# Optimization experiments

Hardware: AMD Instinct MI355X
Metric: run time of the kernel (lower is better)

The kernel has to match this reference:

```python
import math
import jax, jax.numpy as jnp
import numpy as np

# ---------------- static structure (mirrors CG_woFilter_cuda + MyBatchNormWeightMM) ----------------
LMAX = 4
TAUS = [16, 16, 16, 16, 16]          # t_F: input channels per degree l
T_O  = [16, 16, 16, 16, 16]          # output channels per degree l after weight matmul
BN_EPS = 1e-5

# all (l, l1, l2) triples with l2 <= l1 <= lmax and |l1-l2| <= l <= min(l1+l2, lmax), sorted by (l,l1,l2)
TRIPLES = sorted([(l, l1, l2)
                  for l1 in range(LMAX + 1)
                  for l2 in range(l1 + 1)
                  for l in range(l1 - l2, min(l1 + l2, LMAX) + 1)])

T_FF = [0] * (LMAX + 1)              # t_FF[l] = sum over triples of taus[l1]*taus[l2]
for (l, l1, l2) in TRIPLES:
    T_FF[l] += TAUS[l1] * TAUS[l2]

def _cg_coef(j1, m1, j2, m2, j, m):
    """Clebsch-Gordan coefficient <j1 m1 j2 m2 | j m> (Condon-Shortley)."""
    if m1 + m2 != m:
        return 0.0
    f = math.factorial
    if j < abs(j1 - j2) or j > j1 + j2:
        return 0.0
    pref = math.sqrt((2 * j + 1) * f(j + j1 - j2) * f(j - j1 + j2) * f(j1 + j2 - j) / f(j1 + j2 + j + 1))
    pref *= math.sqrt(f(j + m) * f(j - m) * f(j1 - m1) * f(j1 + m1) * f(j2 - m2) * f(j2 + m2))
    s = 0.0
    for k in range(0, j1 + j2 - j + 1):
        if (j1 - m1 - k) < 0 or (j2 + m2 - k) < 0 or (j - j2 + m1 + k) < 0 or (j - j1 - m2 + k) < 0:
            continue
        s += ((-1.0) ** k) / (f(k) * f(j1 + j2 - j - k) * f(j1 - m1 - k)
                              * f(j2 + m2 - k) * f(j - j2 + m1 + k) * f(j - j1 - m2 + k))
    return pref * s

def _cg_matrix(l, l1, l2):
    C = np.zeros((2 * l + 1, 2 * l1 + 1, 2 * l2 + 1), dtype=np.float32)
    for m in range(-l, l + 1):
        for m1 in range(-l1, l1 + 1):
            m2 = m - m1
            if -l2 <= m2 <= l2:
                C[m + l, m1 + l1, m2 + l2] = _cg_coef(l1, m1, l2, m2, l, m)
    return C

CG_MATS = {t: jnp.asarray(_cg_matrix(*t)) for t in TRIPLES}

M_IN = sum(TAUS[l] * (2 * l + 1) for l in range(LMAX + 1))      # 400
W_LEN = sum(T_FF[l] * T_O[l] for l in range(LMAX + 1))          # 172032


def setup_inputs() -> dict:
    key = jax.random.key(0)
    k1, k2 = jax.random.split(key)
    B = 256
    Fs = jax.random.normal(k1, (B, M_IN, 2), dtype=jnp.float32)
    W = jax.random.normal(k2, (W_LEN, 2), dtype=jnp.float32) * 0.05
    return {"Fs": Fs, "W": W}


def reference(Fs, W):
    B = Fs.shape[0]
    # split input into per-degree blocks: F_l [B, tau, 2l+1, 2]
    Fl, off = [], 0
    for l in range(LMAX + 1):
        n = TAUS[l] * (2 * l + 1)
        Fl.append(Fs[:, off:off + n, :].reshape(B, TAUS[l], 2 * l + 1, 2))
        off += n
    # sparse CG tensor product: per-triple complex outer product contracted with CG coefs
    frags = [[] for _ in range(LMAX + 1)]
    for (l, l1, l2) in TRIPLES:
        C = CG_MATS[(l, l1, l2)]                     # [2l+1, 2l1+1, 2l2+1]
        a, b = Fl[l1], Fl[l2]
        ar, ai = a[..., 0], a[..., 1]
        br, bi = b[..., 0], b[..., 1]
        rr = jnp.einsum('bip,bjq,mpq->bijm', ar, br, C)
        ii = jnp.einsum('bip,bjq,mpq->bijm', ai, bi, C)
        ri = jnp.einsum('bip,bjq,mpq->bijm', ar, bi, C)
        ir = jnp.einsum('bip,bjq,mpq->bijm', ai, br, C)
        fr = (rr - ii).reshape(B, -1, 2 * l + 1)     # channels flattened as c1*tau2 + c2 (t_offsets order)
        fi = (ri + ir).reshape(B, -1, 2 * l + 1)
        frags[l].append(jnp.stack([fr, fi], axis=-1))
    # per-degree fragment batchnorm + complex weight matmul (FN_WMM)
    outs, woff = [], 0
    for l in range(LMAX + 1):
        FF = jnp.concatenate(frags[l], axis=1)       # [B, t_FF, 2l+1, 2]
        var = jnp.mean(jnp.sum(FF * FF, axis=-1), axis=(0, 2))      # per-channel mean |z|^2
        FFn = FF / (jnp.sqrt(var)[None, :, None, None] + BN_EPS)
        n = T_FF[l] * T_O[l]
        Wl = W[woff:woff + n].reshape(T_O[l], T_FF[l], 2)
        woff += n
        wr, wi = Wl[..., 0], Wl[..., 1]
        xr, xi = FFn[..., 0], FFn[..., 1]
        yr = jnp.einsum('oc,bcm->bom', wr, xr) - jnp.einsum('oc,bcm->bom', wi, xi)
        yi = jnp.einsum('oc,bcm->bom', wr, xi) + jnp.einsum('oc,bcm->bom', wi, xr)
        outs.append(jnp.stack([yr, yi], axis=-1).reshape(B, T_O[l] * (2 * l + 1), 2))
    return jnp.concatenate(outs, axis=1)             # [B, sum t_O[l]*(2l+1), 2] = [B, 400, 2]
```

## Files before the change

kernel.cpp:

```cpp
#include <hip/hip_runtime.h>
#include <math.h>

#define NTRI 42
#define NCH  10752
#define B_SZ 256
#define AH_PL 172032

typedef float    f32x4 __attribute__((ext_vector_type(4)));
typedef _Float16 half8 __attribute__((ext_vector_type(8)));
typedef _Float16 half4 __attribute__((ext_vector_type(4)));
typedef _Float16 f16x2 __attribute__((ext_vector_type(2)));

constexpr int CT_L [NTRI]={0,0,0,0,0, 1,1,1,1,1,1,1,1, 2,2,2,2,2,2,2,2,2,2, 3,3,3,3,3,3,3,3,3,3, 4,4,4,4,4,4,4,4,4};
constexpr int CT_L1[NTRI]={0,1,2,3,4, 1,1,2,2,3,3,4,4, 1,2,2,2,3,3,3,4,4,4, 2,2,3,3,3,3,4,4,4,4, 2,3,3,3,4,4,4,4,4};
constexpr int CT_L2[NTRI]={0,1,2,3,4, 0,1,1,2,2,3,3,4, 1,0,1,2,1,2,3,2,3,4, 1,2,0,1,2,3,1,2,3,4, 2,1,2,3,0,1,2,3,4};
constexpr int CT_T [NTRI]={0,1,2,3,4, 0,1,2,3,4,5,6,7, 0,1,2,3,4,5,6,7,8,9, 0,1,2,3,4,5,6,7,8,9, 0,1,2,3,4,5,6,7,8};

constexpr int KL_t[5]    ={1280,2048,2560,2560,2304};
constexpr int GBASE_t[5] ={0,1280,3328,5888,8448};
constexpr int ROFF_t[5]  ={0,16,64,144,256};
constexpr int NM_t[5]    ={1,3,5,7,9};
constexpr int FFB_t[5]   ={0,327680,1900544,5177344,9764864};
#define FF_TOT 15073280
constexpr int PL_t[5]    ={0,5,29,79,149};
#define PART_PL 4096
#define PART_TOT (230*PART_PL)

__device__ const int   dCTL[NTRI]={0,0,0,0,0, 1,1,1,1,1,1,1,1, 2,2,2,2,2,2,2,2,2,2, 3,3,3,3,3,3,3,3,3,3, 4,4,4,4,4,4,4,4,4};
__device__ const int   dCTT[NTRI]={0,1,2,3,4, 0,1,2,3,4,5,6,7, 0,1,2,3,4,5,6,7,8,9, 0,1,2,3,4,5,6,7,8,9, 0,1,2,3,4,5,6,7,8};
__device__ const int   dK[5]   ={1280,2048,2560,2560,2304};
__device__ const int   dWOFF[5]={0,20480,53248,94208,135168};
__device__ const int   dNM[5]  ={1,3,5,7,9};
__device__ const int   dFFB[5] ={0,327680,1900544,5177344,9764864};
__device__ const int   dPL[5]  ={0,5,29,79,149};
__device__ const int   dGB[5]  ={0,1280,3328,5888,8448};
__device__ const int   dROFF[5]={0,16,64,144,256};
__device__ const int   dNT[5]  ={5,8,10,10,9};
__device__ const float dINV[5] ={1.f/256.f,1.f/768.f,1.f/1280.f,1.f/1792.f,1.f/2304.f};

__device__ float  g_varsum[NCH];
__device__ __align__(16) f16x2  g_ff[FF_TOT];
__device__ __align__(16) f16x2  g_ah[2*AH_PL];
__device__ float2 g_part[PART_TOT];

constexpr double cfact(int n){ double r=1.0; for(int i=2;i<=n;i++) r*=(double)i; return r; }
constexpr double csqrt_(double v){ double x = v>1.0? v:1.0; for(int i=0;i<80;i++) x = 0.5*(x+v/x); return x; }
constexpr double ccg(int j1,int m1,int j2,int m2,int j,int m){
    if(m1+m2!=m) return 0.0;
    double pref = csqrt_((2.0*j+1.0)*cfact(j+j1-j2)*cfact(j-j1+j2)*cfact(j1+j2-j)/cfact(j1+j2+j+1));
    pref *= csqrt_(cfact(j+m)*cfact(j-m)*cfact(j1-m1)*cfact(j1+m1)*cfact(j2-m2)*cfact(j2+m2));
    double s=0.0;
    for(int k=0;k<=j1+j2-j;k++){
        int a=j1-m1-k, bb=j2+m2-k, c=j-j2+m1+k, d=j-j1-m2+k;
        if(a<0||bb<0||c<0||d<0) continue;
        double term = 1.0/(cfact(k)*cfact(j1+j2-j-k)*cfact(a)*cfact(bb)*cfact(c)*cfact(d));
        s += (k&1)? -term : term;
    }
    return pref*s;
}
struct CG81 { float a[81]; };
constexpr CG81 makecg(int l,int l1,int l2){
    CG81 t{};
    const int n1=2*l1+1;
    for(int mi=0;mi<2*l+1;mi++)
        for(int p=0;p<n1;p++){
            const int m=mi-l, m1=p-l1, m2=m-m1;
            if(m2>=-l2 && m2<=l2) t.a[mi*n1+p]=(float)ccg(l1,m1,l2,m2,l,m);
        }
    return t;
}
template<int TR> struct CGC { static constexpr CG81 t = makecg(CT_L[TR],CT_L1[TR],CT_L2[TR]); };

template<int TR>
__device__ __forceinline__ void cg_pair(const float2* __restrict__ sF,
                                        int i, int j0,
                                        float2* __restrict__ ff0,
                                        float2* __restrict__ ff1){
    constexpr int L=CT_L[TR], L1=CT_L1[TR], L2=CT_L2[TR];
    constexpr int N1=2*L1+1, N2=2*L2+1, NM=2*L+1;
    float2 A[N1], B0[N2], B1[N2];
    #pragma unroll
    for(int p=0;p<N1;p++) A[p]=sF[ROFF_t[L1]+i*N1+p];
    #pragma unroll
    for(int q=0;q<N2;q++) B0[q]=sF[ROFF_t[L2]+j0*N2+q];
    #pragma unroll
    for(int q=0;q<N2;q++) B1[q]=sF[ROFF_t[L2]+(j0+1)*N2+q];
    #pragma unroll
    for(int mi=0;mi<NM;mi++){
        float aR0=0.f, aI0=0.f, aR1=0.f, aI1=0.f;
        const int pLo = (mi-L+L1-L2) > 0 ? (mi-L+L1-L2) : 0;
        const int pHi = (mi-L+L1+L2) < 2*L1 ? (mi-L+L1+L2) : 2*L1;
        #pragma unroll
        for(int p=0;p<N1;p++){
            if(p>=pLo && p<=pHi){
                const float c = CGC<TR>::t.a[mi*N1+p];
                if(c != 0.f){
                    const int q = mi - L - p + L1 + L2;
                    const float cax=c*A[p].x, cay=c*A[p].y;
                    const float2 b0=B0[q], b1=B1[q];
                    aR0 = fmaf(cax,b0.x,aR0); aR0 = fmaf(-cay,b0.y,aR0);
                    aI0 = fmaf(cax,b0.y,aI0); aI0 = fmaf( cay,b0.x,aI0);
                    aR1 = fmaf(cax,b1.x,aR1); aR1 = fmaf(-cay,b1.y,aR1);
                    aI1 = fmaf(cax,b1.y,aI1); aI1 = fmaf( cay,b1.x,aI1);
                }
            }
        }
        ff0[mi]=make_float2(aR0,aI0);
        ff1[mi]=make_float2(aR1,aI1);
    }
}

template<int TR>
__device__ __forceinline__ void cg_one(const float2* __restrict__ sF, int bq, int t){
    constexpr int L=CT_L[TR], NM=2*L+1, T=CT_T[TR], K=KL_t[L];
    constexpr int NMK=NM*K;
    const int half = t>>7, tt = t&127;
    const int ch0 = tt*2;
    const int i = ch0>>4, j0 = ch0&15;
    float n20=0.f, n21=0.f;
    #pragma unroll
    for(int b4=0;b4<4;b4++){
        const int slab = half*4+b4;
        const int b = bq*8 + slab;
        float2 ff0[NM], ff1[NM];
        cg_pair<TR>(sF + slab*400, i, j0, ff0, ff1);
        const int base = FFB_t[L] + b*NMK + T*256 + ch0;
        #pragma unroll
        for(int m=0;m<NM;m++){
            n20 = fmaf(ff0[m].x,ff0[m].x,n20); n20 = fmaf(ff0[m].y,ff0[m].y,n20);
            n21 = fmaf(ff1[m].x,ff1[m].x,n21); n21 = fmaf(ff1[m].y,ff1[m].y,n21);
            half4 h;
            h[0]=(_Float16)ff0[m].x; h[1]=(_Float16)ff0[m].y;
            h[2]=(_Float16)ff1[m].x; h[3]=(_Float16)ff1[m].y;
            *reinterpret_cast<half4*>(g_ff + base + m*K) = h;
        }
    }
    atomicAdd(&g_varsum[GBASE_t[L] + T*256 + ch0    ], n20);
    atomicAdd(&g_varsum[GBASE_t[L] + T*256 + ch0 + 1], n21);
}

template<int TR>
__device__ __forceinline__ void cg_disp(int tr, const float2* sF, int bq, int t){
    if constexpr (TR < NTRI){
        if(tr==TR) cg_one<TR>(sF,bq,t);
        else       cg_disp<TR+1>(tr,sF,bq,t);
    }
}

__global__ void __launch_bounds__(256) k_cg(const float2* __restrict__ Fs){
    __shared__ float4 sF4[1600];
    const int bq=blockIdx.y, t=threadIdx.x;
    const float4* __restrict__ F4 = reinterpret_cast<const float4*>(Fs) + bq*1600;
    #pragma unroll
    for(int k=0;k<6;k++) sF4[t + k*256] = F4[t + k*256];
    if(t<64) sF4[t+1536] = F4[t+1536];
    __syncthreads();
    cg_disp<0>(blockIdx.x, reinterpret_cast<const float2*>(sF4), bq, t);
}

__global__ void __launch_bounds__(256) k_wn(const float2* __restrict__ W2){
    const int tr=blockIdx.x, t=threadIdx.x;
    const int l=dCTL[tr], T=dCTT[tr], K=dK[l];
    const int ch = dGB[l] + T*256 + t;
    const float s = g_varsum[ch];
    g_varsum[ch] = 0.f;
    const float invv = 1.f/(sqrtf(s*dINV[l])+1e-5f);
    const int base = dWOFF[l] + T*256 + t;
    #pragma unroll 4
    for(int o=0;o<16;o++){
        const float2 w = W2[base + o*K];
        f16x2 hr, hi;
        hr.x=(_Float16)( w.x*invv); hr.y=(_Float16)(-w.y*invv);
        hi.x=(_Float16)( w.y*invv); hi.y=(_Float16)( w.x*invv);
        g_ah[base + o*K]         = hr;
        g_ah[AH_PL + base + o*K] = hi;
    }
}

__global__ void __launch_bounds__(256) k_mm(){
    const int j=blockIdx.x;
    const int wv=threadIdx.x>>6, lane=threadIdx.x&63;
    const int slot=blockIdx.y*4+wv;
    const int bgA=slot, bgB=slot+8;
    const int l=(j<5)?0:(j<29)?1:(j<79)?2:(j<149)?3:4;
    const int nm=dNM[l];
    const int loc=j-dPL[l];
    const int T=loc/nm, m=loc-T*nm;
    const int K=dK[l];
    const int l15=lane&15, kg=lane>>4;
    const half8* __restrict__ Arp = reinterpret_cast<const half8*>(g_ah + dWOFF[l] + l15*K + T*256 + kg*4);
    const half8* __restrict__ Aip = reinterpret_cast<const half8*>(g_ah + AH_PL + dWOFF[l] + l15*K + T*256 + kg*4);
    const half8* __restrict__ XpA = reinterpret_cast<const half8*>(g_ff + dFFB[l] + (bgA*16+l15)*(nm*K) + m*K + T*256 + kg*4);
    const half8* __restrict__ XpB = reinterpret_cast<const half8*>(g_ff + dFFB[l] + (bgB*16+l15)*(nm*K) + m*K + T*256 + kg*4);
    f32x4 arA={0.f,0.f,0.f,0.f}, aiA={0.f,0.f,0.f,0.f};
    f32x4 arB={0.f,0.f,0.f,0.f}, aiB={0.f,0.f,0.f,0.f};
    #pragma unroll
    for(int ks=0; ks<16; ks++){
        const half8 Ar = Arp[ks*4];
        const half8 Ai = Aip[ks*4];
        const half8 BA = XpA[ks*4];
        const half8 BB = XpB[ks*4];
        arA = __builtin_amdgcn_mfma_f32_16x16x32_f16(Ar, BA, arA, 0,0,0);
        aiA = __builtin_amdgcn_mfma_f32_16x16x32_f16(Ai, BA, aiA, 0,0,0);
        arB = __builtin_amdgcn_mfma_f32_16x16x32_f16(Ar, BB, arB, 0,0,0);
        aiB = __builtin_amdgcn_mfma_f32_16x16x32_f16(Ai, BB, aiB, 0,0,0);
    }
    float2* __restrict__ ppA = g_part + j*PART_PL + bgA*256;
    float2* __restrict__ ppB = g_part + j*PART_PL + bgB*256;
    #pragma unroll
    for(int r=0;r<4;r++){
        ppA[(kg*4+r)*16 + l15] = make_float2(arA[r], aiA[r]);
        ppB[(kg*4+r)*16 + l15] = make_float2(arB[r], aiB[r]);
    }
}

__global__ void __launch_bounds__(448) k_red(float2* __restrict__ out){
    const int b=blockIdx.x, r=threadIdx.x;
    if(r>=400) return;
    const int l = (r<16)?0:(r<64)?1:(r<144)?2:(r<256)?3:4;
    const int om = r - dROFF[l];
    const int nm = dNM[l];
    const int o = om/nm, m = om - o*nm;
    const float2* __restrict__ pp = g_part + (dPL[l]+m)*PART_PL + (b>>4)*256 + o*16 + (b&15);
    float2 s=make_float2(0.f,0.f);
    const int nt=dNT[l];
    for(int T=0;T<nt;T++){
        const float2 v = pp[T*nm*PART_PL];
        s.x+=v.x; s.y+=v.y;
    }
    out[b*400+r]=s;
}

extern "C" void kernel_launch(void* const* d_in, const int* in_sizes, int n_in,
                              void* d_out, int out_size, void* d_ws, size_t ws_size,
                              hipStream_t stream){
    const float2* Fs = (const float2*)d_in[0];
    const float2* W  = (const float2*)d_in[1];
    float2* out = (float2*)d_out;

    k_cg <<<dim3(NTRI,32), 256, 0, stream>>>(Fs);
    k_wn <<<dim3(NTRI),    256, 0, stream>>>(W);
    k_mm <<<dim3(230,2),   256, 0, stream>>>();
    k_red<<<dim3(B_SZ),    448, 0, stream>>>(out);
}
```

Before: 118.5 us.

## Fold split-K reduction into matmul kernel, drop partial buffer and reduce kernel

The matmul kernel now loops over all K-chunks (T) inside one wave and writes final outputs directly, so the partial-sum buffer and the separate reduction kernel go away. The grid changes from 230x2 blocks of four waves to 25x16 single-wave blocks, each handling one batch group and one m, with two alternating accumulators to hide MFMA latency. This removes one launch and the partial write/read round trip. The cost is far fewer waves (400) with longer serial K loops, which may underuse the GPU.

```diff
diff --git a/kernel.cpp b/kernel.cpp
--- a/kernel.cpp
+++ b/kernel.cpp
@@ -22,9 +22,6 @@
 constexpr int NM_t[5]    ={1,3,5,7,9};
 constexpr int FFB_t[5]   ={0,327680,1900544,5177344,9764864};
 #define FF_TOT 15073280
-constexpr int PL_t[5]    ={0,5,29,79,149};
-#define PART_PL 4096
-#define PART_TOT (230*PART_PL)
 
 __device__ const int   dCTL[NTRI]={0,0,0,0,0, 1,1,1,1,1,1,1,1, 2,2,2,2,2,2,2,2,2,2, 3,3,3,3,3,3,3,3,3,3, 4,4,4,4,4,4,4,4,4};
 __device__ const int   dCTT[NTRI]={0,1,2,3,4, 0,1,2,3,4,5,6,7, 0,1,2,3,4,5,6,7,8,9, 0,1,2,3,4,5,6,7,8,9, 0,1,2,3,4,5,6,7,8};
@@ -32,16 +29,16 @@
 __device__ const int   dWOFF[5]={0,20480,53248,94208,135168};
 __device__ const int   dNM[5]  ={1,3,5,7,9};
 __device__ const int   dFFB[5] ={0,327680,1900544,5177344,9764864};
-__device__ const int   dPL[5]  ={0,5,29,79,149};
 __device__ const int   dGB[5]  ={0,1280,3328,5888,8448};
 __device__ const int   dROFF[5]={0,16,64,144,256};
 __device__ const int   dNT[5]  ={5,8,10,10,9};
 __device__ const float dINV[5] ={1.f/256.f,1.f/768.f,1.f/1280.f,1.f/1792.f,1.f/2304.f};
+__device__ const int   dJL[25]={0, 1,1,1, 2,2,2,2,2, 3,3,3,3,3,3,3, 4,4,4,4,4,4,4,4,4};
+__device__ const int   dJM[25]={0, 0,1,2, 0,1,2,3,4, 0,1,2,3,4,5,6, 0,1,2,3,4,5,6,7,8};
 
 __device__ float  g_varsum[NCH];
 __device__ __align__(16) f16x2  g_ff[FF_TOT];
 __device__ __align__(16) f16x2  g_ah[2*AH_PL];
-__device__ float2 g_part[PART_TOT];
 
 constexpr double cfact(int n){ double r=1.0; for(int i=2;i<=n;i++) r*=(double)i; return r; }
 constexpr double csqrt_(double v){ double x = v>1.0? v:1.0; for(int i=0;i<80;i++) x = 0.5*(x+v/x); return x; }
@@ -177,58 +174,39 @@
     }
 }
 
-__global__ void __launch_bounds__(256) k_mm(){
-    const int j=blockIdx.x;
-    const int wv=threadIdx.x>>6, lane=threadIdx.x&63;
-    const int slot=blockIdx.y*4+wv;
-    const int bgA=slot, bgB=slot+8;
-    const int l=(j<5)?0:(j<29)?1:(j<79)?2:(j<149)?3:4;
-    const int nm=dNM[l];
-    const int loc=j-dPL[l];
-    const int T=loc/nm, m=loc-T*nm;
-    const int K=dK[l];
+__global__ void __launch_bounds__(64) k_mm(float2* __restrict__ out){
+    const int j=blockIdx.x, bg=blockIdx.y;
+    const int l=dJL[j], m=dJM[j];
+    const int nm=dNM[l], K=dK[l], nt=dNT[l];
+    const int lane=threadIdx.x;
     const int l15=lane&15, kg=lane>>4;
-    const half8* __restrict__ Arp = reinterpret_cast<const half8*>(g_ah + dWOFF[l] + l15*K + T*256 + kg*4);
-    const half8* __restrict__ Aip = reinterpret_cast<const half8*>(g_ah + AH_PL + dWOFF[l] + l15*K + T*256 + kg*4);
-    const half8* __restrict__ XpA = reinterpret_cast<const half8*>(g_ff + dFFB[l] + (bgA*16+l15)*(nm*K) + m*K + T*256 + kg*4);
-    const half8* __restrict__ XpB = reinterpret_cast<const half8*>(g_ff + dFFB[l] + (bgB*16+l15)*(nm*K) + m*K + T*256 + kg*4);
-    f32x4 arA={0.f,0.f,0.f,0.f}, aiA={0.f,0.f,0.f,0.f};
-    f32x4 arB={0.f,0.f,0.f,0.f}, aiB={0.f,0.f,0.f,0.f};
-    #pragma unroll
-    for(int ks=0; ks<16; ks++){
-        const half8 Ar = Arp[ks*4];
-        const half8 Ai = Aip[ks*4];
-        const half8 BA = XpA[ks*4];
-        const half8 BB = XpB[ks*4];
-        arA = __builtin_amdgcn_mfma_f32_16x16x32_f16(Ar, BA, arA, 0,0,0);
-        aiA = __builtin_amdgcn_mfma_f32_16x16x32_f16(Ai, BA, aiA, 0,0,0);
-        arB = __builtin_amdgcn_mfma_f32_16x16x32_f16(Ar, BB, arB, 0,0,0);
-        aiB = __builtin_amdgcn_mfma_f32_16x16x32_f16(Ai, BB, aiB, 0,0,0);
-    }
-    float2* __restrict__ ppA = g_part + j*PART_PL + bgA*256;
-    float2* __restrict__ ppB = g_part + j*PART_PL + bgB*256;
+    const half8* __restrict__ Arp = reinterpret_cast<const half8*>(g_ah + dWOFF[l] + l15*K + kg*4);
+    const half8* __restrict__ Aip = reinterpret_cast<const half8*>(g_ah + AH_PL + dWOFF[l] + l15*K + kg*4);
+    const half8* __restrict__ Xp  = reinterpret_cast<const half8*>(g_ff + dFFB[l] + (bg*16+l15)*(nm*K) + m*K + kg*4);
+    f32x4 ar0={0.f,0.f,0.f,0.f}, ar1={0.f,0.f,0.f,0.f};
+    f32x4 ai0={0.f,0.f,0.f,0.f}, ai1={0.f,0.f,0.f,0.f};
+    for(int T=0;T<nt;T++){
+        const int tb = T*64;
+        #pragma unroll
+        for(int ks=0; ks<16; ks++){
+            const half8 Ar = Arp[tb + ks*4];
+            const half8 Ai = Aip[tb + ks*4];
+            const half8 Bf = Xp [tb + ks*4];
+            if(ks & 1){
+                ar1 = __builtin_amdgcn_mfma_f32_16x16x32_f16(Ar, Bf, ar1, 0,0,0);
+                ai1 = __builtin_amdgcn_mfma_f32_16x16x32_f16(Ai, Bf, ai1, 0,0,0);
+            } else {
+                ar0 = __builtin_amdgcn_mfma_f32_16x16x32_f16(Ar, Bf, ar0, 0,0,0);
+                ai0 = __builtin_amdgcn_mfma_f32_16x16x32_f16(Ai, Bf, ai0, 0,0,0);
+            }
+        }
+    }
+    const f32x4 ar = ar0 + ar1, ai = ai0 + ai1;
+    float2* __restrict__ op = out + (bg*16 + l15)*400 + dROFF[l] + m;
     #pragma unroll
     for(int r=0;r<4;r++){
-        ppA[(kg*4+r)*16 + l15] = make_float2(arA[r], aiA[r]);
-        ppB[(kg*4+r)*16 + l15] = make_float2(arB[r], aiB[r]);
-    }
-}
-
-__global__ void __launch_bounds__(448) k_red(float2* __restrict__ out){
-    const int b=blockIdx.x, r=threadIdx.x;
-    if(r>=400) return;
-    const int l = (r<16)?0:(r<64)?1:(r<144)?2:(r<256)?3:4;
-    const int om = r - dROFF[l];
-    const int nm = dNM[l];
-    const int o = om/nm, m = om - o*nm;
-    const float2* __restrict__ pp = g_part + (dPL[l]+m)*PART_PL + (b>>4)*256 + o*16 + (b&15);
-    float2 s=make_float2(0.f,0.f);
-    const int nt=dNT[l];
-    for(int T=0;T<nt;T++){
-        const float2 v = pp[T*nm*PART_PL];
-        s.x+=v.x; s.y+=v.y;
-    }
-    out[b*400+r]=s;
+        op[(kg*4+r)*nm] = make_float2(ar[r], ai[r]);
+    }
 }
 
 extern "C" void kernel_launch(void* const* d_in, const int* in_sizes, int n_in,
@@ -240,6 +218,5 @@
 
     k_cg <<<dim3(NTRI,32), 256, 0, stream>>>(Fs);
     k_wn <<<dim3(NTRI),    256, 0, stream>>>(W);
-    k_mm <<<dim3(230,2),   256, 0, stream>>>();
-    k_red<<<dim3(B_SZ),    448, 0, stream>>>(out);
-}
+    k_mm <<<dim3(25,16),    64, 0, stream>>>(out);
+}
```

After: 129.4 us. 1.09x slower.
